# Performance work log

Measured on AMD Instinct MI355X. Metric: run time of the kernel, lower is better.

## Reference

```python
import jax, jax.numpy as jnp
import numpy as np

DIM = 2048
NUM_HEADS = 16
HEAD_DIM = DIM // NUM_HEADS
ROPE_BASE = 10000.0


def _rope_tables(seq_len, head_dim, dtype):
    # inv_freq over even indices, emb = cat(freqs, freqs) as in RoPEPositionalEncoding
    inv_freq = 1.0 / (ROPE_BASE ** (jnp.arange(0, head_dim, 2, dtype=jnp.float32) / head_dim))
    t = jnp.arange(seq_len, dtype=jnp.float32)
    freqs = jnp.outer(t, inv_freq)                      # [S, D/2]
    emb = jnp.concatenate([freqs, freqs], axis=-1)      # [S, D]
    # add head axis so tables broadcast over [B, S, H, D]
    return jnp.cos(emb)[:, None, :].astype(dtype), jnp.sin(emb)[:, None, :].astype(dtype)


def _apply_rope(x, cos, sin):
    # x: [B, S, H, D]; cos/sin: [S, 1, D]
    x1, x2 = x[..., ::2], x[..., 1::2]
    rotated = jnp.concatenate([-x2, x1], axis=-1)
    return x * cos + rotated * sin


def setup_inputs() -> dict:
    key = jax.random.key(0)
    ks = jax.random.split(key, 5)
    B, S = 2, 2048
    s = 1.0 / np.sqrt(DIM)
    return {
        "x": jax.random.normal(ks[0], (B, S, DIM), dtype=jnp.float32),
        "Wq": jax.random.normal(ks[1], (DIM, DIM), dtype=jnp.float32) * s,
        "Wk": jax.random.normal(ks[2], (DIM, DIM), dtype=jnp.float32) * s,
        "Wv": jax.random.normal(ks[3], (DIM, DIM), dtype=jnp.float32) * s,
        "Wo": jax.random.normal(ks[4], (DIM, DIM), dtype=jnp.float32) * s,
    }


def reference(x, Wq, Wk, Wv, Wo):
    B, S, _ = x.shape
    H, D = NUM_HEADS, HEAD_DIM
    scale = D ** -0.5

    q = (x @ Wq.T).reshape(B, S, H, D)
    k = (x @ Wk.T).reshape(B, S, H, D)
    v = (x @ Wv.T).reshape(B, S, H, D)

    cos, sin = _rope_tables(S, D, x.dtype)
    q = _apply_rope(q, cos, sin)
    k = _apply_rope(k, cos, sin)

    # [B, H, S, D]
    q = q.transpose(0, 2, 1, 3)
    k = k.transpose(0, 2, 1, 3)
    v = v.transpose(0, 2, 1, 3)

    scores = jnp.einsum("bhqd,bhkd->bhqk", q, k) * scale
    causal = jnp.tril(jnp.ones((S, S), dtype=bool))
    scores = jnp.where(causal, scores, -jnp.inf)
    attn = jax.nn.softmax(scores, axis=-1)

    out = jnp.einsum("bhqk,bhkd->bhqd", attn, v)
    out = out.transpose(0, 2, 1, 3).reshape(B, S, H * D)
    return out @ Wo.T
```

## Files before the change

### kernel.cpp

```cpp
#include <hip/hip_runtime.h>
#include <math.h>

#define DIM   2048
#define NH    16
#define HD    128
#define BB    2
#define SS    2048
#define MTOT  4096

typedef unsigned short u16;
typedef short bf16x8 __attribute__((ext_vector_type(8)));
typedef float f32x4  __attribute__((ext_vector_type(4)));

typedef const void __attribute__((address_space(1)))* gas_ptr;
typedef void __attribute__((address_space(3)))* las_ptr;

__device__ __forceinline__ u16 f2bf(float f){
  union { float f; unsigned u; } v; v.f = f;
  unsigned r = v.u + 0x7FFFu + ((v.u >> 16) & 1u);
  return (u16)(r >> 16);
}
__device__ __forceinline__ float bf2f(u16 h){
  union { unsigned u; float f; } v; v.u = ((unsigned)h) << 16;
  return v.f;
}

__global__ __launch_bounds__(256) void cvt_kernel(const float* __restrict__ in,
                                                  u16* __restrict__ out, int n4){
  int i = blockIdx.x * blockDim.x + threadIdx.x;
  if (i >= n4) return;
  float4 v = ((const float4*)in)[i];
  ushort4 o;
  o.x = f2bf(v.x); o.y = f2bf(v.y); o.z = f2bf(v.z); o.w = f2bf(v.w);
  ((ushort4*)out)[i] = o;
}

template<bool STORE_BF16>
__global__ __launch_bounds__(256) void gemm_bt(
    const u16* __restrict__ A,
    const u16* __restrict__ B0, const u16* __restrict__ B1, const u16* __restrict__ B2,
    void* __restrict__ C0, void* __restrict__ C1, void* __restrict__ C2,
    int M, int N, int K)
{
  const u16* Bm = (blockIdx.z == 0) ? B0 : (blockIdx.z == 1 ? B1 : B2);
  void* Cm      = (blockIdx.z == 0) ? C0 : (blockIdx.z == 1 ? C1 : C2);

  __shared__ __align__(16) u16 Alds[128 * 32];
  __shared__ __align__(16) u16 Blds[128 * 32];

  const int tid  = threadIdx.x;
  const int lane = tid & 63;
  const int wave = tid >> 6;
  const int wr   = wave >> 1;
  const int wc   = wave & 1;
  const int lg   = lane >> 4;
  const int lr   = lane & 15;
  const int m0   = blockIdx.y * 128;
  const int n0   = blockIdx.x * 128;

  f32x4 acc[4][4];
#pragma unroll
  for (int m = 0; m < 4; ++m)
#pragma unroll
    for (int n = 0; n < 4; ++n) acc[m][n] = (f32x4)0.0f;

  for (int k0 = 0; k0 < K; k0 += 32) {
    __syncthreads();
#pragma unroll
    for (int it = 0; it < 2; ++it) {
      int chunk = it * 256 + tid;
      int row   = chunk >> 2;
      int cc    = chunk & 3;
      const u16* ga = A  + (size_t)(m0 + row) * K + k0 + cc * 8;
      const u16* gb = Bm + (size_t)(n0 + row) * K + k0 + cc * 8;
      char* la = (char*)Alds + (it * 256 + wave * 64) * 16;
      char* lb = (char*)Blds + (it * 256 + wave * 64) * 16;
      __builtin_amdgcn_global_load_lds((gas_ptr)ga, (las_ptr)la, 16, 0, 0);
      __builtin_amdgcn_global_load_lds((gas_ptr)gb, (las_ptr)lb, 16, 0, 0);
    }
    __syncthreads();

    bf16x8 a[4], b[4];
#pragma unroll
    for (int m = 0; m < 4; ++m)
      a[m] = *(const bf16x8*)(Alds + (wr * 64 + m * 16 + lr) * 32 + lg * 8);
#pragma unroll
    for (int n = 0; n < 4; ++n)
      b[n] = *(const bf16x8*)(Blds + (wc * 64 + n * 16 + lr) * 32 + lg * 8);
#pragma unroll
    for (int m = 0; m < 4; ++m)
#pragma unroll
      for (int n = 0; n < 4; ++n)
        acc[m][n] = __builtin_amdgcn_mfma_f32_16x16x32_bf16(a[m], b[n], acc[m][n], 0, 0, 0);
  }

#pragma unroll
  for (int m = 0; m < 4; ++m) {
    int grow = m0 + wr * 64 + m * 16 + lg * 4;
#pragma unroll
    for (int n = 0; n < 4; ++n) {
      int gcol = n0 + wc * 64 + n * 16 + lr;
#pragma unroll
      for (int r = 0; r < 4; ++r) {
        float val = acc[m][n][r];
        if (STORE_BF16) ((u16*)Cm)[(size_t)(grow + r) * N + gcol]   = f2bf(val);
        else            ((float*)Cm)[(size_t)(grow + r) * N + gcol] = val;
      }
    }
  }
}

__global__ __launch_bounds__(256) void rope_kernel(u16* __restrict__ Q, u16* __restrict__ Kt){
  int gid  = blockIdx.x * 4 + (threadIdx.x >> 6);
  int lane = threadIdx.x & 63;
  int h = gid & (NH - 1);
  int s = (gid >> 4) & (SS - 1);
  int b = gid >> 15;
  size_t base = ((size_t)(b * SS + s)) * DIM + (size_t)h * HD;

  float ang = (float)s * __expf(-(float)lane * 0.14391156831212787f);
  float c, sn;
  sincosf(ang, &sn, &c);
  int jh = lane >> 1;
  int par = lane & 1;

  unsigned pq = *(const unsigned*)(Q + base + 2 * lane);
  float qe = bf2f((u16)(pq & 0xffff)), qo = bf2f((u16)(pq >> 16));
  float qa  = __shfl(qe, jh),      qb  = __shfl(qo, jh);
  float qa2 = __shfl(qe, 32 + jh), qb2 = __shfl(qo, 32 + jh);
  float qxj   = par ? qb  : qa;
  float qxj64 = par ? qb2 : qa2;
  u16 q_lo = f2bf(qxj   * c - qo * sn);
  u16 q_hi = f2bf(qxj64 * c + qe * sn);

  unsigned pk = *(const unsigned*)(Kt + base + 2 * lane);
  float ke = bf2f((u16)(pk & 0xffff)), ko = bf2f((u16)(pk >> 16));
  float ka  = __shfl(ke, jh),      kb  = __shfl(ko, jh);
  float ka2 = __shfl(ke, 32 + jh), kb2 = __shfl(ko, 32 + jh);
  float kxj   = par ? kb  : ka;
  float kxj64 = par ? kb2 : ka2;
  u16 k_lo = f2bf(kxj   * c - ko * sn);
  u16 k_hi = f2bf(kxj64 * c + ke * sn);

  Q [base + lane] = q_lo;  Q [base + 64 + lane] = q_hi;
  Kt[base + lane] = k_lo;  Kt[base + 64 + lane] = k_hi;
}

__global__ __launch_bounds__(256) void transpose_v(const u16* __restrict__ V,
                                                   u16* __restrict__ VT){
  __shared__ __align__(16) u16 T[64 * 64];
  const int tid = threadIdx.x;
  const int s0 = blockIdx.x * 64;
  const int d0 = blockIdx.y * 64;
  const int bh = blockIdx.z;
  const int b = bh >> 4, h = bh & 15;

#pragma unroll
  for (int it = 0; it < 2; ++it) {
    int c = it * 256 + tid;
    int s = c >> 3, cc = c & 7;
    uint4 v = *(const uint4*)(V + (size_t)(b * SS + s0 + s) * DIM + h * HD + d0 + cc * 8);
    *(uint4*)((char*)T + s * 128 + (((cc ^ (s & 7)) & 7) << 4)) = v;
  }
  __syncthreads();
#pragma unroll
  for (int it = 0; it < 2; ++it) {
    int c = it * 256 + tid;
    int d = c >> 3, sc = c & 7;
    u16 tmp[8];
#pragma unroll
    for (int j = 0; j < 8; ++j) {
      int s = sc * 8 + j;
      tmp[j] = *(const u16*)((char*)T + s * 128 + ((((d >> 3) ^ (s & 7)) & 7) << 4) + (d & 7) * 2);
    }
    *(uint4*)(VT + (size_t)bh * HD * SS + (size_t)(d0 + d) * SS + s0 + sc * 8) = *(const uint4*)tmp;
  }
}

#define SCALE 0.08838834764831845f

__global__ __launch_bounds__(512) void attn_kernel(
    const u16* __restrict__ Q, const u16* __restrict__ Kg, const u16* __restrict__ VT,
    u16* __restrict__ AO)
{
  __shared__ __align__(16) u16 Klds[2][64 * 128];
  __shared__ __align__(16) u16 Vlds[2][128 * 64];
  __shared__ __align__(16) u16 Plds[8][16 * 64];

  const int tid  = threadIdx.x;
  const int lane = tid & 63;
  const int w    = tid >> 6;
  const int lg   = lane >> 4;
  const int lr   = lane & 15;
  const int pair = blockIdx.x;
  const int bh   = blockIdx.y;
  const int b    = bh >> 4, h = bh & 15;
  const size_t headoff = (size_t)b * SS * DIM + (size_t)h * HD;
  const u16* VTh = VT + (size_t)bh * HD * SS;

  for (int half = 0; half < 2; ++half) {
    const int Qt = half ? (15 - pair) : pair;
    const int qbase = Qt * 128;
    const int nkv = Qt * 2 + 2;

    bf16x8 qf[4];
    {
      const u16* qrow = Q + headoff + (size_t)(qbase + w * 16 + lr) * DIM;
#pragma unroll
      for (int kf = 0; kf < 4; ++kf)
        qf[kf] = *(const bf16x8*)(qrow + kf * 32 + lg * 8);
    }

    f32x4 o_acc[8];
#pragma unroll
    for (int nf = 0; nf < 8; ++nf) o_acc[nf] = (f32x4)0.0f;
    float mrow[4] = {-INFINITY, -INFINITY, -INFINITY, -INFINITY};
    float lrow[4] = {0.f, 0.f, 0.f, 0.f};

    int cur = 0;

#define STAGE(BUF, T)                                                              \
    {                                                                              \
      const int kv0s = (T) * 64;                                                   \
      _Pragma("unroll")                                                            \
      for (int it = 0; it < 2; ++it) {                                             \
        int c = it * 512 + tid;                                                    \
        int r = c >> 4, slot = c & 15;                                             \
        int cc = slot ^ (r & 7);                                                   \
        const u16* ga = Kg + headoff + (size_t)(kv0s + r) * DIM + cc * 8;          \
        char* la = (char*)Klds[BUF] + (it * 512 + w * 64) * 16;                    \
        __builtin_amdgcn_global_load_lds((gas_ptr)ga, (las_ptr)la, 16, 0, 0);      \
      }                                                                            \
      _Pragma("unroll")                                                            \
      for (int it = 0; it < 2; ++it) {                                             \
        int c = it * 512 + tid;                                                    \
        int d = c >> 3, slot = c & 7;                                              \
        int cc = slot ^ (d & 7);                                                   \
        const u16* gv = VTh + (size_t)d * SS + kv0s + cc * 8;                      \
        char* lv = (char*)Vlds[BUF] + (it * 512 + w * 64) * 16;                    \
        __builtin_amdgcn_global_load_lds((gas_ptr)gv, (las_ptr)lv, 16, 0, 0);      \
      }                                                                            \
    }

    STAGE(0, 0);
    __syncthreads();

    for (int t = 0; t < nkv; ++t) {
      const int kv0 = t * 64;
      if (t + 1 < nkv) STAGE(cur ^ 1, t + 1);

      if (kv0 <= qbase + w * 16 + 15) {
        f32x4 sacc[4];
#pragma unroll
        for (int sf = 0; sf < 4; ++sf) {
          sacc[sf] = (f32x4)0.0f;
          int row = sf * 16 + lr;
          int sw = row & 7;
#pragma unroll
          for (int kf = 0; kf < 4; ++kf) {
            int cc = kf * 4 + lg;
            bf16x8 kfrag = *(const bf16x8*)((char*)Klds[cur] + row * 256 + ((cc ^ sw) << 4));
            sacc[sf] = __builtin_amdgcn_mfma_f32_16x16x32_bf16(qf[kf], kfrag, sacc[sf], 0, 0, 0);
          }
        }

        float p[4][4];
        float mt[4];
#pragma unroll
        for (int r = 0; r < 4; ++r) {
          int qrow = qbase + w * 16 + lg * 4 + r;
          float mx = -INFINITY;
#pragma unroll
          for (int sf = 0; sf < 4; ++sf) {
            float v = sacc[sf][r] * SCALE;
            if (kv0 + sf * 16 + lr > qrow) v = -INFINITY;
            p[sf][r] = v;
            mx = fmaxf(mx, v);
          }
          mx = fmaxf(mx, __shfl_xor(mx, 1));
          mx = fmaxf(mx, __shfl_xor(mx, 2));
          mx = fmaxf(mx, __shfl_xor(mx, 4));
          mx = fmaxf(mx, __shfl_xor(mx, 8));
          mt[r] = mx;
        }
        float alpha[4];
#pragma unroll
        for (int r = 0; r < 4; ++r) {
          float mn = fmaxf(mrow[r], mt[r]);
          alpha[r] = __expf(mrow[r] - mn);
          mrow[r] = mn;
        }
#pragma unroll
        for (int r = 0; r < 4; ++r) {
          float s = 0.f;
#pragma unroll
          for (int sf = 0; sf < 4; ++sf) {
            float pv = __expf(p[sf][r] - mrow[r]);
            p[sf][r] = pv;
            s += pv;
          }
          s += __shfl_xor(s, 1);
          s += __shfl_xor(s, 2);
          s += __shfl_xor(s, 4);
          s += __shfl_xor(s, 8);
          lrow[r] = lrow[r] * alpha[r] + s;
        }
#pragma unroll
        for (int nf = 0; nf < 8; ++nf)
#pragma unroll
          for (int r = 0; r < 4; ++r) o_acc[nf][r] *= alpha[r];

#pragma unroll
        for (int sf = 0; sf < 4; ++sf)
#pragma unroll
          for (int r = 0; r < 4; ++r) {
            int row = lg * 4 + r, col = sf * 16 + lr;
            int byteoff = (row * 128 + col * 2) ^ ((row & 7) << 4);
            *(u16*)((char*)Plds[w] + byteoff) = f2bf(p[sf][r]);
          }

#pragma unroll
        for (int ks = 0; ks < 2; ++ks) {
          bf16x8 pfrag = *(const bf16x8*)((char*)Plds[w] + ((lr * 128 + ks * 64 + lg * 16) ^ ((lr & 7) << 4)));
#pragma unroll
          for (int nf = 0; nf < 8; ++nf) {
            int vrow = nf * 16 + lr;
            int cc = ks * 4 + lg;
            bf16x8 vfrag = *(const bf16x8*)((char*)Vlds[cur] + vrow * 128 + ((cc ^ (vrow & 7)) << 4));
            o_acc[nf] = __builtin_amdgcn_mfma_f32_16x16x32_bf16(pfrag, vfrag, o_acc[nf], 0, 0, 0);
          }
        }
      }

      __syncthreads();
      cur ^= 1;
    }

    float inv[4];
#pragma unroll
    for (int r = 0; r < 4; ++r) inv[r] = 1.0f / lrow[r];
#pragma unroll
    for (int nf = 0; nf < 8; ++nf)
#pragma unroll
      for (int r = 0; r < 4; ++r) {
        int grow = qbase + w * 16 + lg * 4 + r;
        int col  = nf * 16 + lr;
        AO[(size_t)(b * SS + grow) * DIM + h * HD + col] = f2bf(o_acc[nf][r] * inv[r]);
      }
#undef STAGE
  }
}

extern "C" void kernel_launch(void* const* d_in, const int* in_sizes, int n_in,
                              void* d_out, int out_size, void* d_ws, size_t ws_size,
                              hipStream_t stream)
{
  const float* x  = (const float*)d_in[0];
  const float* Wq = (const float*)d_in[1];
  const float* Wk = (const float*)d_in[2];
  const float* Wv = (const float*)d_in[3];
  const float* Wo = (const float*)d_in[4];
  float* out = (float*)d_out;

  char* ws = (char*)d_ws;
  const size_t XB_BYTES = (size_t)MTOT * DIM * 2;
  const size_t W_BYTES  = (size_t)DIM * DIM * 2;
  u16* xb = (u16*)ws;
  u16* w0 = (u16*)(ws + XB_BYTES);
  u16* w1 = (u16*)(ws + XB_BYTES + W_BYTES);
  u16* w2 = (u16*)(ws + XB_BYTES + 2 * W_BYTES);
  u16* Qb = (u16*)(ws + XB_BYTES + 3 * W_BYTES);
  u16* Kb = Qb + (size_t)MTOT * DIM;
  u16* Vb = Kb + (size_t)MTOT * DIM;
  u16* AO = xb;
  u16* VTb = w1;

  cvt_kernel<<<8192, 256, 0, stream>>>(x,  xb, 2097152);
  cvt_kernel<<<4096, 256, 0, stream>>>(Wq, w0, 1048576);
  cvt_kernel<<<4096, 256, 0, stream>>>(Wk, w1, 1048576);
  cvt_kernel<<<4096, 256, 0, stream>>>(Wv, w2, 1048576);

  gemm_bt<true><<<dim3(16, 32, 3), 256, 0, stream>>>(xb, w0, w1, w2,
                                                     (void*)Qb, (void*)Kb, (void*)Vb,
                                                     MTOT, DIM, DIM);

  transpose_v<<<dim3(32, 2, 32), 256, 0, stream>>>(Vb, VTb);

  rope_kernel<<<16384, 256, 0, stream>>>(Qb, Kb);

  cvt_kernel<<<4096, 256, 0, stream>>>(Wo, w0, 1048576);

  attn_kernel<<<dim3(8, 32), 512, 0, stream>>>(Qb, Kb, VTb, AO);

  gemm_bt<false><<<dim3(16, 32, 1), 256, 0, stream>>>(AO, w0, w0, w0,
                                                      (void*)out, (void*)out, (void*)out,
                                                      MTOT, DIM, DIM);
}
```

Measured before the change: 448.5 us.

## Replace GEMMs with 256x256 double-buffered pipelined kernel and fuse input conversions

Replaces the 128x128 single-buffered projection GEMM with a 256x256-tile, 512-thread kernel that double-buffers LDS over a K step of 64. It interleaves async global-to-LDS loads with MFMA phases using explicit waitcnt, barriers and setprio. It also remaps workgroup IDs across XCD groups for locality, and merges the four fp32-to-bf16 conversion launches into one. The goal is to hide memory latency and raise MFMA utilisation. The trade-off is large LDS use (128KB per block), higher register pressure, and fragile hand-tuned synchronisation.

```diff
diff --git a/kernel.cpp b/kernel.cpp
--- a/kernel.cpp
+++ b/kernel.cpp
@@ -7,6 +7,7 @@
 #define BB    2
 #define SS    2048
 #define MTOT  4096
+#define NT    32
 
 typedef unsigned short u16;
 typedef short bf16x8 __attribute__((ext_vector_type(8)));
@@ -23,6 +24,26 @@
 __device__ __forceinline__ float bf2f(u16 h){
   union { unsigned u; float f; } v; v.u = ((unsigned)h) << 16;
   return v.f;
+}
+
+__global__ __launch_bounds__(256) void cvt_all(
+    const float* __restrict__ x,  const float* __restrict__ wq,
+    const float* __restrict__ wk, const float* __restrict__ wv,
+    u16* __restrict__ xb, u16* __restrict__ w0, u16* __restrict__ w1, u16* __restrict__ w2){
+  int i = blockIdx.x * 256 + threadIdx.x;
+  const float* src; u16* dst; int j;
+  if (i < 2097152) { src = x; dst = xb; j = i; }
+  else {
+    int k = i - 2097152;
+    int seg = k >> 20;
+    j = k & 1048575;
+    src = (seg == 0) ? wq : (seg == 1 ? wk : wv);
+    dst = (seg == 0) ? w0 : (seg == 1 ? w1 : w2);
+  }
+  float4 v = ((const float4*)src)[j];
+  ushort4 o;
+  o.x = f2bf(v.x); o.y = f2bf(v.y); o.z = f2bf(v.z); o.w = f2bf(v.w);
+  ((ushort4*)dst)[j] = o;
 }
 
 __global__ __launch_bounds__(256) void cvt_kernel(const float* __restrict__ in,
@@ -36,75 +57,133 @@
 }
 
 template<bool STORE_BF16>
-__global__ __launch_bounds__(256) void gemm_bt(
+__global__ __launch_bounds__(512, 2) void gemm256(
     const u16* __restrict__ A,
     const u16* __restrict__ B0, const u16* __restrict__ B1, const u16* __restrict__ B2,
-    void* __restrict__ C0, void* __restrict__ C1, void* __restrict__ C2,
-    int M, int N, int K)
+    void* __restrict__ C0, void* __restrict__ C1, void* __restrict__ C2)
 {
-  const u16* Bm = (blockIdx.z == 0) ? B0 : (blockIdx.z == 1 ? B1 : B2);
-  void* Cm      = (blockIdx.z == 0) ? C0 : (blockIdx.z == 1 ? C1 : C2);
-
-  __shared__ __align__(16) u16 Alds[128 * 32];
-  __shared__ __align__(16) u16 Blds[128 * 32];
+  __shared__ __align__(16) u16 Ar[2][2][256 * 32];
+  __shared__ __align__(16) u16 Br[2][2][256 * 32];
 
   const int tid  = threadIdx.x;
   const int lane = tid & 63;
   const int wave = tid >> 6;
-  const int wr   = wave >> 1;
-  const int wc   = wave & 1;
+  const int wm   = wave >> 2;
+  const int wn   = wave & 3;
   const int lg   = lane >> 4;
   const int lr   = lane & 15;
-  const int m0   = blockIdx.y * 128;
-  const int n0   = blockIdx.x * 128;
-
-  f32x4 acc[4][4];
-#pragma unroll
-  for (int m = 0; m < 4; ++m)
+
+  const int cpx = gridDim.x >> 3;
+  const int wg  = (blockIdx.x & 7) * cpx + (blockIdx.x >> 3);
+  const int z   = wg >> 7;
+  const int rem = wg & 127;
+  const int m0  = (rem >> 3) * 256;
+  const int n0  = (rem & 7) * 256;
+
+  const u16* Bm = (z == 0) ? B0 : (z == 1 ? B1 : B2);
+  void* Cm      = (z == 0) ? C0 : (z == 1 ? C1 : C2);
+  const u16* Asrc = A  + (size_t)m0 * DIM;
+  const u16* Bsrc = Bm + (size_t)n0 * DIM;
+
+  f32x4 acc[8][4];
+#pragma unroll
+  for (int m = 0; m < 8; ++m)
 #pragma unroll
     for (int n = 0; n < 4; ++n) acc[m][n] = (f32x4)0.0f;
-
-  for (int k0 = 0; k0 < K; k0 += 32) {
-    __syncthreads();
+  bf16x8 breg[4];
+
+  auto stage = [&](const u16* src, u16* ldsreg, int kabs) {
 #pragma unroll
     for (int it = 0; it < 2; ++it) {
-      int chunk = it * 256 + tid;
-      int row   = chunk >> 2;
-      int cc    = chunk & 3;
-      const u16* ga = A  + (size_t)(m0 + row) * K + k0 + cc * 8;
-      const u16* gb = Bm + (size_t)(n0 + row) * K + k0 + cc * 8;
-      char* la = (char*)Alds + (it * 256 + wave * 64) * 16;
-      char* lb = (char*)Blds + (it * 256 + wave * 64) * 16;
-      __builtin_amdgcn_global_load_lds((gas_ptr)ga, (las_ptr)la, 16, 0, 0);
-      __builtin_amdgcn_global_load_lds((gas_ptr)gb, (las_ptr)lb, 16, 0, 0);
-    }
-    __syncthreads();
-
-    bf16x8 a[4], b[4];
-#pragma unroll
-    for (int m = 0; m < 4; ++m)
-      a[m] = *(const bf16x8*)(Alds + (wr * 64 + m * 16 + lr) * 32 + lg * 8);
-#pragma unroll
-    for (int n = 0; n < 4; ++n)
-      b[n] = *(const bf16x8*)(Blds + (wc * 64 + n * 16 + lr) * 32 + lg * 8);
-#pragma unroll
-    for (int m = 0; m < 4; ++m)
-#pragma unroll
-      for (int n = 0; n < 4; ++n)
-        acc[m][n] = __builtin_amdgcn_mfma_f32_16x16x32_bf16(a[m], b[n], acc[m][n], 0, 0, 0);
-  }
-
-#pragma unroll
-  for (int m = 0; m < 4; ++m) {
-    int grow = m0 + wr * 64 + m * 16 + lg * 4;
-#pragma unroll
-    for (int n = 0; n < 4; ++n) {
-      int gcol = n0 + wc * 64 + n * 16 + lr;
+      int c   = it * 512 + tid;
+      int st  = c >> 4;
+      int row = ((st >> 2) << 4) + (c & 15);
+      int k   = kabs + ((st & 3) << 3);
+      const u16* g = src + (size_t)row * DIM + k;
+      char* l = (char*)ldsreg + (it * 512 + wave * 64) * 16;
+      __builtin_amdgcn_global_load_lds((gas_ptr)g, (las_ptr)l, 16, 0, 0);
+    }
+  };
+
+  stage(Asrc, Ar[0][0], 0);
+  stage(Bsrc, Br[0][0], 0);
+  stage(Asrc, Ar[0][1], 32);
+  stage(Bsrc, Br[0][1], 32);
+  asm volatile("s_waitcnt vmcnt(4)" ::: "memory");
+  __builtin_amdgcn_s_barrier();
+
+#define GPHASE(QQ, KK, GG)                                                              \
+  {                                                                                     \
+    const u16* Ab_ = Ar[b][KK];                                                         \
+    const u16* Bb_ = Br[b][KK];                                                         \
+    bf16x8 a0 = *(const bf16x8*)((const char*)Ab_ + ((((wm*8 + GG*4 + 0)*4 + lg) << 8) + (lr << 4))); \
+    bf16x8 a1 = *(const bf16x8*)((const char*)Ab_ + ((((wm*8 + GG*4 + 1)*4 + lg) << 8) + (lr << 4))); \
+    bf16x8 a2 = *(const bf16x8*)((const char*)Ab_ + ((((wm*8 + GG*4 + 2)*4 + lg) << 8) + (lr << 4))); \
+    bf16x8 a3 = *(const bf16x8*)((const char*)Ab_ + ((((wm*8 + GG*4 + 3)*4 + lg) << 8) + (lr << 4))); \
+    if (GG == 0) {                                                                      \
+      _Pragma("unroll")                                                                 \
+      for (int n_ = 0; n_ < 4; ++n_)                                                    \
+        breg[n_] = *(const bf16x8*)((const char*)Bb_ + ((((wn*4 + n_)*4 + lg) << 8) + (lr << 4))); \
+    }                                                                                   \
+    if (t + 1 < NT) {                                                                   \
+      if (QQ == 0) stage(Asrc, Ar[b ^ 1][0], (t + 1) * 64);                             \
+      if (QQ == 1) stage(Bsrc, Br[b ^ 1][0], (t + 1) * 64);                             \
+      if (QQ == 2) stage(Asrc, Ar[b ^ 1][1], (t + 1) * 64 + 32);                        \
+      if (QQ == 3) stage(Bsrc, Br[b ^ 1][1], (t + 1) * 64 + 32);                        \
+    }                                                                                   \
+    __builtin_amdgcn_s_barrier();                                                       \
+    asm volatile("s_waitcnt lgkmcnt(0)" ::: "memory");                                  \
+    __builtin_amdgcn_sched_barrier(0);                                                  \
+    __builtin_amdgcn_s_setprio(1);                                                      \
+    {                                                                                   \
+      acc[GG*4+0][0] = __builtin_amdgcn_mfma_f32_16x16x32_bf16(a0, breg[0], acc[GG*4+0][0], 0,0,0); \
+      acc[GG*4+0][1] = __builtin_amdgcn_mfma_f32_16x16x32_bf16(a0, breg[1], acc[GG*4+0][1], 0,0,0); \
+      acc[GG*4+0][2] = __builtin_amdgcn_mfma_f32_16x16x32_bf16(a0, breg[2], acc[GG*4+0][2], 0,0,0); \
+      acc[GG*4+0][3] = __builtin_amdgcn_mfma_f32_16x16x32_bf16(a0, breg[3], acc[GG*4+0][3], 0,0,0); \
+      acc[GG*4+1][0] = __builtin_amdgcn_mfma_f32_16x16x32_bf16(a1, breg[0], acc[GG*4+1][0], 0,0,0); \
+      acc[GG*4+1][1] = __builtin_amdgcn_mfma_f32_16x16x32_bf16(a1, breg[1], acc[GG*4+1][1], 0,0,0); \
+      acc[GG*4+1][2] = __builtin_amdgcn_mfma_f32_16x16x32_bf16(a1, breg[2], acc[GG*4+1][2], 0,0,0); \
+      acc[GG*4+1][3] = __builtin_amdgcn_mfma_f32_16x16x32_bf16(a1, breg[3], acc[GG*4+1][3], 0,0,0); \
+      acc[GG*4+2][0] = __builtin_amdgcn_mfma_f32_16x16x32_bf16(a2, breg[0], acc[GG*4+2][0], 0,0,0); \
+      acc[GG*4+2][1] = __builtin_amdgcn_mfma_f32_16x16x32_bf16(a2, breg[1], acc[GG*4+2][1], 0,0,0); \
+      acc[GG*4+2][2] = __builtin_amdgcn_mfma_f32_16x16x32_bf16(a2, breg[2], acc[GG*4+2][2], 0,0,0); \
+      acc[GG*4+2][3] = __builtin_amdgcn_mfma_f32_16x16x32_bf16(a2, breg[3], acc[GG*4+2][3], 0,0,0); \
+      acc[GG*4+3][0] = __builtin_amdgcn_mfma_f32_16x16x32_bf16(a3, breg[0], acc[GG*4+3][0], 0,0,0); \
+      acc[GG*4+3][1] = __builtin_amdgcn_mfma_f32_16x16x32_bf16(a3, breg[1], acc[GG*4+3][1], 0,0,0); \
+      acc[GG*4+3][2] = __builtin_amdgcn_mfma_f32_16x16x32_bf16(a3, breg[2], acc[GG*4+3][2], 0,0,0); \
+      acc[GG*4+3][3] = __builtin_amdgcn_mfma_f32_16x16x32_bf16(a3, breg[3], acc[GG*4+3][3], 0,0,0); \
+    }                                                                                   \
+    __builtin_amdgcn_s_setprio(0);                                                      \
+    if (QQ == 1) {                                                                      \
+      if (t + 1 < NT) { asm volatile("s_waitcnt vmcnt(4)" ::: "memory"); }              \
+      else            { asm volatile("s_waitcnt vmcnt(0)" ::: "memory"); }              \
+    }                                                                                   \
+    if (QQ == 3) {                                                                      \
+      if (t + 1 < NT) { asm volatile("s_waitcnt vmcnt(4)" ::: "memory"); }              \
+    }                                                                                   \
+    __builtin_amdgcn_s_barrier();                                                       \
+  }
+
+  for (int t = 0; t < NT; ++t) {
+    const int b = t & 1;
+    GPHASE(0, 0, 0)
+    GPHASE(1, 0, 1)
+    GPHASE(2, 1, 0)
+    GPHASE(3, 1, 1)
+  }
+#undef GPHASE
+
+#pragma unroll
+  for (int mf = 0; mf < 8; ++mf) {
+    int grow = m0 + wm * 128 + mf * 16 + lg * 4;
+#pragma unroll
+    for (int nf = 0; nf < 4; ++nf) {
+      int gcol = n0 + wn * 64 + nf * 16 + lr;
 #pragma unroll
       for (int r = 0; r < 4; ++r) {
-        float val = acc[m][n][r];
-        if (STORE_BF16) ((u16*)Cm)[(size_t)(grow + r) * N + gcol]   = f2bf(val);
-        else            ((float*)Cm)[(size_t)(grow + r) * N + gcol] = val;
+        float val = acc[mf][nf][r];
+        if (STORE_BF16) ((u16*)Cm)[(size_t)(grow + r) * DIM + gcol]   = f2bf(val);
+        else            ((float*)Cm)[(size_t)(grow + r) * DIM + gcol] = val;
       }
     }
   }
@@ -375,14 +454,10 @@
   u16* AO = xb;
   u16* VTb = w1;
 
-  cvt_kernel<<<8192, 256, 0, stream>>>(x,  xb, 2097152);
-  cvt_kernel<<<4096, 256, 0, stream>>>(Wq, w0, 1048576);
-  cvt_kernel<<<4096, 256, 0, stream>>>(Wk, w1, 1048576);
-  cvt_kernel<<<4096, 256, 0, stream>>>(Wv, w2, 1048576);
-
-  gemm_bt<true><<<dim3(16, 32, 3), 256, 0, stream>>>(xb, w0, w1, w2,
-                                                     (void*)Qb, (void*)Kb, (void*)Vb,
-                                                     MTOT, DIM, DIM);
+  cvt_all<<<20480, 256, 0, stream>>>(x, Wq, Wk, Wv, xb, w0, w1, w2);
+
+  gemm256<true><<<dim3(384), 512, 0, stream>>>(xb, w0, w1, w2,
+                                               (void*)Qb, (void*)Kb, (void*)Vb);
 
   transpose_v<<<dim3(32, 2, 32), 256, 0, stream>>>(Vb, VTb);
 
@@ -392,7 +467,6 @@
 
   attn_kernel<<<dim3(8, 32), 512, 0, stream>>>(Qb, Kb, VTb, AO);
 
-  gemm_bt<false><<<dim3(16, 32, 1), 256, 0, stream>>>(AO, w0, w0, w0,
-                                                      (void*)out, (void*)out, (void*)out,
-                                                      MTOT, DIM, DIM);
-}
+  gemm256<false><<<dim3(128), 512, 0, stream>>>(AO, w0, w0, w0,
+                                                (void*)out, (void*)out, (void*)out);
+}
```

Result: slower. 489.4 us (+9.1%).

## Double-buffer GEMM LDS tiles, swizzle the LDS layout, and fuse input conversions

Applied to the files above, without the earlier changes.

The GEMM now keeps two LDS buffers and issues the global-to-LDS loads for the next K tile before the MFMA work on the current one, so there is one barrier per iteration instead of two. The LDS layout is reordered so each 16-row by 8-column fragment is contiguous, which changes how the loads are addressed and is meant to cut bank conflicts. The four separate fp32-to-bf16 conversion launches are merged into a single kernel. LDS use doubles, which can lower occupancy.

```diff
diff --git a/kernel.cpp b/kernel.cpp
--- a/kernel.cpp
+++ b/kernel.cpp
@@ -23,6 +23,26 @@
 __device__ __forceinline__ float bf2f(u16 h){
   union { unsigned u; float f; } v; v.u = ((unsigned)h) << 16;
   return v.f;
+}
+
+__global__ __launch_bounds__(256) void cvt_all(
+    const float* __restrict__ x,  const float* __restrict__ wq,
+    const float* __restrict__ wk, const float* __restrict__ wv,
+    u16* __restrict__ xb, u16* __restrict__ w0, u16* __restrict__ w1, u16* __restrict__ w2){
+  int i = blockIdx.x * 256 + threadIdx.x;
+  const float* src; u16* dst; int j;
+  if (i < 2097152) { src = x; dst = xb; j = i; }
+  else {
+    int k = i - 2097152;
+    int seg = k >> 20;
+    j = k & 1048575;
+    src = (seg == 0) ? wq : (seg == 1 ? wk : wv);
+    dst = (seg == 0) ? w0 : (seg == 1 ? w1 : w2);
+  }
+  float4 v = ((const float4*)src)[j];
+  ushort4 o;
+  o.x = f2bf(v.x); o.y = f2bf(v.y); o.z = f2bf(v.z); o.w = f2bf(v.w);
+  ((ushort4*)dst)[j] = o;
 }
 
 __global__ __launch_bounds__(256) void cvt_kernel(const float* __restrict__ in,
@@ -45,8 +65,8 @@
   const u16* Bm = (blockIdx.z == 0) ? B0 : (blockIdx.z == 1 ? B1 : B2);
   void* Cm      = (blockIdx.z == 0) ? C0 : (blockIdx.z == 1 ? C1 : C2);
 
-  __shared__ __align__(16) u16 Alds[128 * 32];
-  __shared__ __align__(16) u16 Blds[128 * 32];
+  __shared__ __align__(16) u16 Alds[2][4096];
+  __shared__ __align__(16) u16 Blds[2][4096];
 
   const int tid  = threadIdx.x;
   const int lane = tid & 63;
@@ -58,40 +78,51 @@
   const int m0   = blockIdx.y * 128;
   const int n0   = blockIdx.x * 128;
 
+  const u16* Asrc = A  + (size_t)m0 * K;
+  const u16* Bsrc = Bm + (size_t)n0 * K;
+
   f32x4 acc[4][4];
 #pragma unroll
   for (int m = 0; m < 4; ++m)
 #pragma unroll
     for (int n = 0; n < 4; ++n) acc[m][n] = (f32x4)0.0f;
 
-  for (int k0 = 0; k0 < K; k0 += 32) {
-    __syncthreads();
+  auto stageAB = [&](int buf, int k0) {
 #pragma unroll
     for (int it = 0; it < 2; ++it) {
-      int chunk = it * 256 + tid;
-      int row   = chunk >> 2;
-      int cc    = chunk & 3;
-      const u16* ga = A  + (size_t)(m0 + row) * K + k0 + cc * 8;
-      const u16* gb = Bm + (size_t)(n0 + row) * K + k0 + cc * 8;
-      char* la = (char*)Alds + (it * 256 + wave * 64) * 16;
-      char* lb = (char*)Blds + (it * 256 + wave * 64) * 16;
+      int d   = it * 256 + tid;
+      int row = ((d >> 6) << 4) + (d & 15);
+      int kk  = ((d >> 4) & 3) << 3;
+      const u16* ga = Asrc + (size_t)row * K + k0 + kk;
+      const u16* gb = Bsrc + (size_t)row * K + k0 + kk;
+      char* la = (char*)Alds[buf] + (it * 256 + wave * 64) * 16;
+      char* lb = (char*)Blds[buf] + (it * 256 + wave * 64) * 16;
       __builtin_amdgcn_global_load_lds((gas_ptr)ga, (las_ptr)la, 16, 0, 0);
       __builtin_amdgcn_global_load_lds((gas_ptr)gb, (las_ptr)lb, 16, 0, 0);
     }
-    __syncthreads();
+  };
+
+  stageAB(0, 0);
+  __syncthreads();
+
+  for (int k0 = 0; k0 < K; k0 += 32) {
+    const int buf = (k0 >> 5) & 1;
+    if (k0 + 32 < K) stageAB(buf ^ 1, k0 + 32);
 
     bf16x8 a[4], b[4];
 #pragma unroll
     for (int m = 0; m < 4; ++m)
-      a[m] = *(const bf16x8*)(Alds + (wr * 64 + m * 16 + lr) * 32 + lg * 8);
+      a[m] = *(const bf16x8*)((const char*)Alds[buf] + ((((wr * 4 + m) * 4 + lg) << 8) + (lr << 4)));
 #pragma unroll
     for (int n = 0; n < 4; ++n)
-      b[n] = *(const bf16x8*)(Blds + (wc * 64 + n * 16 + lr) * 32 + lg * 8);
+      b[n] = *(const bf16x8*)((const char*)Blds[buf] + ((((wc * 4 + n) * 4 + lg) << 8) + (lr << 4)));
 #pragma unroll
     for (int m = 0; m < 4; ++m)
 #pragma unroll
       for (int n = 0; n < 4; ++n)
         acc[m][n] = __builtin_amdgcn_mfma_f32_16x16x32_bf16(a[m], b[n], acc[m][n], 0, 0, 0);
+
+    __syncthreads();
   }
 
 #pragma unroll
@@ -375,10 +406,7 @@
   u16* AO = xb;
   u16* VTb = w1;
 
-  cvt_kernel<<<8192, 256, 0, stream>>>(x,  xb, 2097152);
-  cvt_kernel<<<4096, 256, 0, stream>>>(Wq, w0, 1048576);
-  cvt_kernel<<<4096, 256, 0, stream>>>(Wk, w1, 1048576);
-  cvt_kernel<<<4096, 256, 0, stream>>>(Wv, w2, 1048576);
+  cvt_all<<<20480, 256, 0, stream>>>(x, Wq, Wk, Wv, xb, w0, w1, w2);
 
   gemm_bt<true><<<dim3(16, 32, 3), 256, 0, stream>>>(xb, w0, w1, w2,
                                                      (void*)Qb, (void*)Kb, (void*)Vb,
```

Result: slower. 499.2 us (+11.3%).
